# Kernel optimization log

Measured on AMD Instinct MI355X. Metric: run time of the kernel, lower is better.

## Reference

```python
import jax, jax.numpy as jnp
import numpy as np

B, C, D, H = 16, 64, 512, 8
SEQ_LEN, LABEL_LEN, PRED_LEN = 1024, 512, 512
DEC_LEN = LABEL_LEN + PRED_LEN
DFF, KSIZE, FACTOR = 2048, 25, 3
E_LAYERS, D_LAYERS = 2, 1


def _pos_emb(L, d):
    pos = np.arange(L, dtype=np.float32)[:, None]
    div = np.exp(np.arange(0, d, 2, dtype=np.float32) * (-np.log(10000.0) / d))
    pe = np.zeros((L, d), np.float32)
    pe[:, 0::2] = np.sin(pos * div)
    pe[:, 1::2] = np.cos(pos * div)
    return jnp.asarray(pe)


def moving_mean(x, k=KSIZE):
    # AvgPool1d(k, stride=1) with replicate padding of (k-1)//2 at both ends
    pad = (k - 1) // 2
    xp = jnp.concatenate([jnp.repeat(x[:, :1], pad, 1), x, jnp.repeat(x[:, -1:], pad, 1)], axis=1)
    cs = jnp.cumsum(xp, axis=1)
    cs = jnp.concatenate([jnp.zeros_like(cs[:, :1]), cs], axis=1)
    return (cs[:, k:] - cs[:, :-k]) / k


def series_decomp(x):
    mm = moving_mean(x)
    return x - mm, mm


def circ_conv3(x, W):
    # Conv1d kernel=3, circular padding=1, no bias. x [B,L,Cin], W [3,Cin,Cout]
    L = x.shape[1]
    xp = jnp.concatenate([x[:, -1:], x, x[:, :1]], axis=1)
    return sum(jnp.einsum('blc,cd->bld', xp[:, k:k + L], W[k]) for k in range(3))


def my_layernorm(x, g, b):
    # LayerNorm then subtract per-sample mean over the time axis (special seasonal layernorm)
    mu = x.mean(-1, keepdims=True)
    var = x.var(-1, keepdims=True)
    xh = (x - mu) / jnp.sqrt(var + 1e-5) * g + b
    return xh - xh.mean(axis=1, keepdims=True)


def autocorrelation(q, k, v):
    # q,k,v: [B,L,H,E]. FFT cross-correlation, top-k lag selection, time-delay aggregation.
    L = q.shape[1]
    qf = jnp.fft.rfft(q.transpose(0, 2, 3, 1), axis=-1)
    kf = jnp.fft.rfft(k.transpose(0, 2, 3, 1), axis=-1)
    corr = jnp.fft.irfft(qf * jnp.conj(kf), n=L, axis=-1)  # [B,H,E,L]
    top_k = int(FACTOR * np.log(L))
    w, delay = jax.lax.top_k(corr.mean(axis=(1, 2)), top_k)  # [B,K]
    tc = jax.nn.softmax(w, axis=-1)
    vp = v.transpose(0, 2, 3, 1)  # [B,H,E,L]
    base = jnp.arange(L)
    agg = jnp.zeros_like(vp)
    for i in range(top_k):  # small fixed K (= int(factor*log L) = 20)
        idx = (base[None, :] + delay[:, i:i + 1]) % L  # circular shift == gather on doubled values
        pattern = jnp.take_along_axis(vp, idx[:, None, None, :], axis=-1)
        agg = agg + pattern * tc[:, i][:, None, None, None]
    return agg.transpose(0, 3, 1, 2)  # [B,L,H,E]


def ac_layer(q_in, kv_in, Wq, bq, Wk, bk, Wv, bv, Wo, bo):
    Bb, L, _ = q_in.shape
    S = kv_in.shape[1]
    E = D // H
    q = (q_in @ Wq + bq).reshape(Bb, L, H, E)
    k = (kv_in @ Wk + bk).reshape(Bb, S, H, E)
    v = (kv_in @ Wv + bv).reshape(Bb, S, H, E)
    out = autocorrelation(q, k, v)  # L == S by construction here
    return out.reshape(Bb, L, D) @ Wo + bo


def _forward(x_enc, x_dec, enc_emb_w, dec_emb_w, enc_Wq, enc_bq, enc_Wk, enc_bk, enc_Wv, enc_bv, enc_Wo, enc_bo, enc_ff1, enc_ff2, enc_ng, enc_nb, dsa_Wq, dsa_bq, dsa_Wk, dsa_bk, dsa_Wv, dsa_bv, dsa_Wo, dsa_bo, dca_Wq, dca_bq, dca_Wk, dca_bk, dca_Wv, dca_bv, dca_Wo, dca_bo, dec_ff1, dec_ff2, dec_trend_w, proj_w, proj_b):
    mean = jnp.repeat(x_enc.mean(axis=1, keepdims=True), PRED_LEN, axis=1)
    zeros = jnp.zeros((x_dec.shape[0], PRED_LEN, x_dec.shape[2]), x_enc.dtype)
    seasonal_init, trend_init = series_decomp(x_enc)
    trend = jnp.concatenate([trend_init[:, -LABEL_LEN:], mean], axis=1)
    seasonal_init = jnp.concatenate([seasonal_init[:, -LABEL_LEN:], zeros], axis=1)
    # encoder (DataEmbedding_wo_temp = token circular conv + sinusoidal pos, dropout=0)
    x = circ_conv3(x_enc, enc_emb_w) + _pos_emb(SEQ_LEN, D)[None]
    for l in range(E_LAYERS):
        x = x + ac_layer(x, x, enc_Wq[l], enc_bq[l], enc_Wk[l], enc_bk[l], enc_Wv[l], enc_bv[l], enc_Wo[l], enc_bo[l])
        x, _ = series_decomp(x)
        y = jax.nn.gelu(x @ enc_ff1[l], approximate=False) @ enc_ff2[l]
        x, _ = series_decomp(x + y)
    enc_out = my_layernorm(x, enc_ng, enc_nb)
    # decoder
    xd = circ_conv3(seasonal_init, dec_emb_w) + _pos_emb(DEC_LEN, D)[None]
    for l in range(D_LAYERS):
        xd = xd + ac_layer(xd, xd, dsa_Wq[l], dsa_bq[l], dsa_Wk[l], dsa_bk[l], dsa_Wv[l], dsa_bv[l], dsa_Wo[l], dsa_bo[l])
        xd, t1 = series_decomp(xd)
        xd = xd + ac_layer(xd, enc_out, dca_Wq[l], dca_bq[l], dca_Wk[l], dca_bk[l], dca_Wv[l], dca_bv[l], dca_Wo[l], dca_bo[l])
        xd, t2 = series_decomp(xd)
        y = jax.nn.gelu(xd @ dec_ff1[l], approximate=False) @ dec_ff2[l]
        xd, t3 = series_decomp(xd + y)
        trend = trend + circ_conv3(t1 + t2 + t3, dec_trend_w[l])  # trend projection conv
    seasonal = xd @ proj_w + proj_b
    out = trend + seasonal
    return out[:, -PRED_LEN:]


def setup_inputs():
    key = jax.random.key(0)
    ks = iter(jax.random.split(key, 64))
    def n(shape, s=0.02):
        return jax.random.normal(next(ks), shape, jnp.float32) * s
    inp = {}
    inp['x_enc'] = jax.random.normal(next(ks), (B, SEQ_LEN, C), jnp.float32)
    inp['x_dec'] = jax.random.normal(next(ks), (B, DEC_LEN, C), jnp.float32)
    inp['enc_emb_w'] = n((3, C, D))
    inp['dec_emb_w'] = n((3, C, D))
    for p in ['Wq', 'Wk', 'Wv', 'Wo']:
        bp = p.replace('W', 'b')
        inp['enc_' + p] = n((E_LAYERS, D, D)); inp['enc_' + bp] = jnp.zeros((E_LAYERS, D))
        inp['dsa_' + p] = n((D_LAYERS, D, D)); inp['dsa_' + bp] = jnp.zeros((D_LAYERS, D))
        inp['dca_' + p] = n((D_LAYERS, D, D)); inp['dca_' + bp] = jnp.zeros((D_LAYERS, D))
    inp['enc_ff1'] = n((E_LAYERS, D, DFF)); inp['enc_ff2'] = n((E_LAYERS, DFF, D))
    inp['enc_ng'] = jnp.ones((D,), jnp.float32); inp['enc_nb'] = jnp.zeros((D,), jnp.float32)
    inp['dec_ff1'] = n((D_LAYERS, D, DFF)); inp['dec_ff2'] = n((D_LAYERS, DFF, D))
    inp['dec_trend_w'] = n((D_LAYERS, 3, D, C))
    inp['proj_w'] = n((D, C)); inp['proj_b'] = jnp.zeros((C,), jnp.float32)
    return inp


def reference(x_enc, x_dec, enc_emb_w, dec_emb_w, enc_Wq, enc_bq, enc_Wk, enc_bk, enc_Wv, enc_bv, enc_Wo, enc_bo, enc_ff1, enc_ff2, enc_ng, enc_nb, dsa_Wq, dsa_bq, dsa_Wk, dsa_bk, dsa_Wv, dsa_bv, dsa_Wo, dsa_bo, dca_Wq, dca_bq, dca_Wk, dca_bk, dca_Wv, dca_bv, dca_Wo, dca_bo, dec_ff1, dec_ff2, dec_trend_w, proj_w, proj_b):
    return _forward(x_enc, x_dec, enc_emb_w, dec_emb_w, enc_Wq, enc_bq, enc_Wk, enc_bk, enc_Wv, enc_bv, enc_Wo, enc_bo, enc_ff1, enc_ff2, enc_ng, enc_nb, dsa_Wq, dsa_bq, dsa_Wk, dsa_bk, dsa_Wv, dsa_bv, dsa_Wo, dsa_bo, dca_Wq, dca_bq, dca_Wk, dca_bk, dca_Wv, dca_bv, dca_Wo, dca_bo, dec_ff1, dec_ff2, dec_trend_w, proj_w, proj_b)
```

## Files before the change

### kernel.cpp

```cpp
#include <hip/hip_runtime.h>
#include <math.h>

#define B_   16
#define L_   1024
#define C_   64
#define D_   512
#define DFF_ 2048
#define TOPK_ 20

typedef float f4 __attribute__((ext_vector_type(4)));
typedef float f32x4 __attribute__((ext_vector_type(4)));
typedef short bf16x8 __attribute__((ext_vector_type(8)));
typedef unsigned short u16x8 __attribute__((ext_vector_type(8)));

__device__ __forceinline__ unsigned short f2bf(float f) {
    union { float f; unsigned u; } a; a.f = f;
    unsigned r = a.u + 0x7fff + ((a.u >> 16) & 1);
    return (unsigned short)(r >> 16);
}
__device__ __forceinline__ float bf2f(unsigned short h) {
    union { unsigned u; float f; } a; a.u = ((unsigned)h) << 16;
    return a.f;
}

__device__ __forceinline__ float gelu_fast(float c) {
    float z  = c * 0.70710678118654752f;
    float az = fabsf(z);
    float t  = __builtin_amdgcn_rcpf(fmaf(0.3275911f, az, 1.0f));
    float p  = fmaf(fmaf(fmaf(fmaf(1.061405429f, t, -1.453152027f), t,
                              1.421413741f), t, -0.284496736f), t, 0.254829592f) * t;
    float e  = __expf(-z * z);
    float ea = fmaf(-p, e, 1.0f);
    float er = copysignf(ea, z);
    return 0.5f * c * (1.0f + er);
}

__device__ __forceinline__ void gld16(const void* g, void* l) {
    __builtin_amdgcn_global_load_lds(
        (const __attribute__((address_space(1))) unsigned int*)g,
        (__attribute__((address_space(3))) unsigned int*)l, 16, 0, 0);
}


__global__ __launch_bounds__(256)
void gemm_bf16(const unsigned short* __restrict__ A, const unsigned short* __restrict__ Bt,
               float* __restrict__ Cf, unsigned short* __restrict__ Cb,
               unsigned short* __restrict__ Cl,
               const float* __restrict__ bias, int M, int N, int K, int flags, int nx)
{
    __shared__ unsigned short As0[128 * 32], As1[128 * 32];
    __shared__ unsigned short Bs0[128 * 32], Bs1[128 * 32];
    const int tid = threadIdx.x;
    const int wave = tid >> 6, lane = tid & 63;

    int total = gridDim.x;
    int h = blockIdx.x;
    int lidx = h;
    if ((total & 7) == 0) {
        int q = total >> 3;
        lidx = (h & 7) * q + (h >> 3);
    }
    const int bm = (lidx / nx) * 128, bn = (lidx % nx) * 128;
    const int wm = (wave >> 1) << 6, wn = (wave & 1) << 6;

    const int r0 = (wave << 5) + (lane >> 2);
    const int kq = (((lane & 3) ^ ((lane >> 3) & 3)) << 3);
    const unsigned short* Ap0 = A + (size_t)(bm + r0) * K + kq;
    const unsigned short* Ap1 = Ap0 + (size_t)16 * K;
    const unsigned short* Bp0 = Bt + (size_t)(bn + r0) * K + kq;
    const unsigned short* Bp1 = Bp0 + (size_t)16 * K;
    const int wo0 = (wave << 5) * 32, wo1 = ((wave << 5) + 16) * 32;

    const int la = lane & 15, h4 = lane >> 4;
    const int sw = (la >> 1) & 3;
    f32x4 acc[4][4] = {};

    for (int k0 = 0; k0 < K; k0 += 64) {
        gld16(Ap0 + k0, &As0[wo0]);      gld16(Ap1 + k0, &As0[wo1]);
        gld16(Bp0 + k0, &Bs0[wo0]);      gld16(Bp1 + k0, &Bs0[wo1]);
        gld16(Ap0 + k0 + 32, &As1[wo0]); gld16(Ap1 + k0 + 32, &As1[wo1]);
        gld16(Bp0 + k0 + 32, &Bs1[wo0]); gld16(Bp1 + k0 + 32, &Bs1[wo1]);
        __syncthreads();
        bf16x8 a[4], b[4];
#pragma unroll
        for (int i = 0; i < 4; ++i) {
            a[i] = *(const bf16x8*)&As0[(wm + i * 16 + la) * 32 + ((h4 ^ sw) << 3)];
            b[i] = *(const bf16x8*)&Bs0[(wn + i * 16 + la) * 32 + ((h4 ^ sw) << 3)];
        }
#pragma unroll
        for (int mi = 0; mi < 4; ++mi)
#pragma unroll
            for (int ni = 0; ni < 4; ++ni)
                acc[mi][ni] = __builtin_amdgcn_mfma_f32_16x16x32_bf16(a[mi], b[ni], acc[mi][ni], 0, 0, 0);
#pragma unroll
        for (int i = 0; i < 4; ++i) {
            a[i] = *(const bf16x8*)&As1[(wm + i * 16 + la) * 32 + ((h4 ^ sw) << 3)];
            b[i] = *(const bf16x8*)&Bs1[(wn + i * 16 + la) * 32 + ((h4 ^ sw) << 3)];
        }
#pragma unroll
        for (int mi = 0; mi < 4; ++mi)
#pragma unroll
            for (int ni = 0; ni < 4; ++ni)
                acc[mi][ni] = __builtin_amdgcn_mfma_f32_16x16x32_bf16(a[mi], b[ni], acc[mi][ni], 0, 0, 0);
        __syncthreads();
    }

#pragma unroll
    for (int mi = 0; mi < 4; ++mi) {
#pragma unroll
        for (int r = 0; r < 4; ++r) {
            int m = bm + wm + mi * 16 + h4 * 4 + r;
#pragma unroll
            for (int ni = 0; ni < 4; ++ni) {
                int n = bn + wn + ni * 16 + la;
                float c = acc[mi][ni][r];
                if (bias) c += bias[n];
                if (flags & 2) c = gelu_fast(c);
                size_t o = (size_t)m * N + n;
                if (Cf) { if (flags & 1) Cf[o] += c; else Cf[o] = c; }
                if (Cb) {
                    unsigned short hb = f2bf(c);
                    Cb[o] = hb;
                    if (Cl) Cl[o] = f2bf(c - bf2f(hb));
                }
            }
        }
    }
}

__global__ __launch_bounds__(256)
void gemm_split(const unsigned short* __restrict__ A, const unsigned short* __restrict__ Bt,
                unsigned short* __restrict__ o0h, unsigned short* __restrict__ o0l, const float* __restrict__ b0,
                unsigned short* __restrict__ o1h, unsigned short* __restrict__ o1l, const float* __restrict__ b1,
                unsigned short* __restrict__ o2h, unsigned short* __restrict__ o2l, const float* __restrict__ b2,
                float* __restrict__ Gz, int M, int N, int K, int nx)
{
    __shared__ unsigned short As0[128 * 32], As1[128 * 32];
    __shared__ unsigned short Bs0[128 * 32], Bs1[128 * 32];
    const int tid = threadIdx.x;
    const int wave = tid >> 6, lane = tid & 63;

    int total = gridDim.x;
    int h = blockIdx.x;
    if (Gz && h < 64) Gz[h * 256 + tid] = 0.f;
    int lidx = h;
    if ((total & 7) == 0) {
        int q = total >> 3;
        lidx = (h & 7) * q + (h >> 3);
    }
    const int bm = (lidx / nx) * 128, bn = (lidx % nx) * 128;
    const int wm = (wave >> 1) << 6, wn = (wave & 1) << 6;

    const int sel = bn >> 9;
    unsigned short* oh = sel == 0 ? o0h : (sel == 1 ? o1h : o2h);
    unsigned short* ol = sel == 0 ? o0l : (sel == 1 ? o1l : o2l);
    const float* bias  = sel == 0 ? b0  : (sel == 1 ? b1  : b2);
    const int nb = bn & 511;

    const int r0 = (wave << 5) + (lane >> 2);
    const int kq = (((lane & 3) ^ ((lane >> 3) & 3)) << 3);
    const unsigned short* Ap0 = A + (size_t)(bm + r0) * K + kq;
    const unsigned short* Ap1 = Ap0 + (size_t)16 * K;
    const unsigned short* Bp0 = Bt + (size_t)(bn + r0) * K + kq;
    const unsigned short* Bp1 = Bp0 + (size_t)16 * K;
    const int wo0 = (wave << 5) * 32, wo1 = ((wave << 5) + 16) * 32;

    const int la = lane & 15, h4 = lane >> 4;
    const int sw = (la >> 1) & 3;
    f32x4 acc[4][4] = {};

    for (int k0 = 0; k0 < K; k0 += 64) {
        gld16(Ap0 + k0, &As0[wo0]);      gld16(Ap1 + k0, &As0[wo1]);
        gld16(Bp0 + k0, &Bs0[wo0]);      gld16(Bp1 + k0, &Bs0[wo1]);
        gld16(Ap0 + k0 + 32, &As1[wo0]); gld16(Ap1 + k0 + 32, &As1[wo1]);
        gld16(Bp0 + k0 + 32, &Bs1[wo0]); gld16(Bp1 + k0 + 32, &Bs1[wo1]);
        __syncthreads();
        bf16x8 a[4], b[4];
#pragma unroll
        for (int i = 0; i < 4; ++i) {
            a[i] = *(const bf16x8*)&As0[(wm + i * 16 + la) * 32 + ((h4 ^ sw) << 3)];
            b[i] = *(const bf16x8*)&Bs0[(wn + i * 16 + la) * 32 + ((h4 ^ sw) << 3)];
        }
#pragma unroll
        for (int mi = 0; mi < 4; ++mi)
#pragma unroll
            for (int ni = 0; ni < 4; ++ni)
                acc[mi][ni] = __builtin_amdgcn_mfma_f32_16x16x32_bf16(a[mi], b[ni], acc[mi][ni], 0, 0, 0);
#pragma unroll
        for (int i = 0; i < 4; ++i) {
            a[i] = *(const bf16x8*)&As1[(wm + i * 16 + la) * 32 + ((h4 ^ sw) << 3)];
            b[i] = *(const bf16x8*)&Bs1[(wn + i * 16 + la) * 32 + ((h4 ^ sw) << 3)];
        }
#pragma unroll
        for (int mi = 0; mi < 4; ++mi)
#pragma unroll
            for (int ni = 0; ni < 4; ++ni)
                acc[mi][ni] = __builtin_amdgcn_mfma_f32_16x16x32_bf16(a[mi], b[ni], acc[mi][ni], 0, 0, 0);
        __syncthreads();
    }

#pragma unroll
    for (int mi = 0; mi < 4; ++mi) {
#pragma unroll
        for (int r = 0; r < 4; ++r) {
            int m = bm + wm + mi * 16 + h4 * 4 + r;
#pragma unroll
            for (int ni = 0; ni < 4; ++ni) {
                int n2 = nb + wn + ni * 16 + la;
                float c = acc[mi][ni][r] + bias[n2];
                size_t o = (size_t)m * 512 + n2;
                unsigned short hb = f2bf(c);
                oh[o] = hb;
                if (ol) ol[o] = f2bf(c - bf2f(hb));
            }
        }
    }
}

__global__ __launch_bounds__(256)
void tcast_kernel(const float* __restrict__ W, unsigned short* __restrict__ Wt, int R, int Cc)
{
    __shared__ float t[32][33];
    int bx = blockIdx.x * 32, by = blockIdx.y * 32;
    int tx = threadIdx.x & 31, ty = threadIdx.x >> 5;
#pragma unroll
    for (int i = 0; i < 32; i += 8)
        t[ty + i][tx] = W[(size_t)(by + ty + i) * Cc + bx + tx];
    __syncthreads();
#pragma unroll
    for (int i = 0; i < 32; i += 8)
        Wt[(size_t)(bx + ty + i) * R + by + tx] = f2bf(t[tx][ty + i]);
}

struct P16 { const float* p[16]; };
__global__ __launch_bounds__(256)
void tcast_all(P16 srcs, unsigned short* __restrict__ dst)
{
    __shared__ float t[32][33];
    const float* W = srcs.p[blockIdx.z];
    unsigned short* Wt = dst + (size_t)blockIdx.z * 262144;
    int bx = blockIdx.x * 32, by = blockIdx.y * 32;
    int tx = threadIdx.x & 31, ty = threadIdx.x >> 5;
#pragma unroll
    for (int i = 0; i < 32; i += 8)
        t[ty + i][tx] = W[(size_t)(by + ty + i) * 512 + bx + tx];
    __syncthreads();
#pragma unroll
    for (int i = 0; i < 32; i += 8)
        Wt[(size_t)(bx + ty + i) * 512 + by + tx] = f2bf(t[tx][ty + i]);
}

__global__ __launch_bounds__(256)
void emb_kernel(const float* __restrict__ A, const float* __restrict__ W,
                float* __restrict__ Xo, unsigned short* __restrict__ Xb)
{
    __shared__ float As[66][68];
    __shared__ float Ws[3][64][64];
    const int tid = threadIdx.x;
    const int bn = blockIdx.x * 64, bm = blockIdx.y * 64;
    const int base = bm & ~1023;
    for (int i = tid; i < 66 * 64; i += 256) {
        int r = i >> 6, c = i & 63;
        int l = (bm - base) + r - 1;
        if (l < 0) l += 1024; else if (l >= 1024) l -= 1024;
        As[r][c] = A[(size_t)(base + l) * 64 + c];
    }
    for (int i = tid; i < 3 * 64 * 64; i += 256) {
        int tap = i >> 12, rem = i & 4095, k = rem >> 6, c = rem & 63;
        Ws[tap][k][c] = W[((size_t)tap * 64 + k) * 512 + bn + c];
    }
    __syncthreads();
    const int tx = tid & 15, ty = tid >> 4;
    float acc[4][4] = {};
    for (int tap = 0; tap < 3; ++tap)
        for (int k = 0; k < 64; ++k) {
            f4 bv = *(const f4*)&Ws[tap][k][tx * 4];
#pragma unroll
            for (int i = 0; i < 4; ++i) {
                float a = As[ty * 4 + i + tap][k];
#pragma unroll
                for (int j = 0; j < 4; ++j)
                    acc[i][j] = fmaf(a, bv[j], acc[i][j]);
            }
        }
#pragma unroll
    for (int i = 0; i < 4; ++i) {
        int m = bm + ty * 4 + i;
        int l = m & 1023;
#pragma unroll
        for (int j = 0; j < 4; ++j) {
            int n = bn + tx * 4 + j;
            float c = acc[i][j];
            int i2 = n & ~1;
            float div = expf(-(float)i2 * 0.017988946039015984f);
            float ang = (float)l * div;
            c += (n & 1) ? cosf(ang) : sinf(ang);
            size_t o = (size_t)m * 512 + n;
            Xo[o] = c;
            Xb[o] = f2bf(c);
        }
    }
}

__global__ __launch_bounds__(256)
void tail_kernel(const float* __restrict__ TSUM, const float* __restrict__ T1,
                 const float* __restrict__ Wt, const float* __restrict__ pw,
                 float* __restrict__ PC, float* __restrict__ PP)
{
    __shared__ float Ts[18][17];
    __shared__ float T1s[16][17];
    __shared__ float Ws[3][16][64];
    __shared__ float Ps[16][64];
    const int tid = threadIdx.x;
    const int bo = blockIdx.x * 16;
    const int kc = blockIdx.y;
    const int b = bo >> 9;
    const int lbase = (bo & 511) + 512;
    const size_t rowbase = (size_t)b << 10;
    const int tc4 = (tid & 15) * 4;
    const int tr = tid >> 4;
    const int kbeg = kc * 64, kend = kbeg + 64;
    float cacc[4] = {}, pacc[4] = {};

    for (int k0 = kbeg; k0 < kend; k0 += 16) {
        for (int i = tid; i < 18 * 16; i += 256) {
            int r = i >> 4, c = i & 15;
            int l = lbase + r - 1; if (l >= 1024) l -= 1024;
            Ts[r][c] = TSUM[(rowbase + l) * 512 + k0 + c];
        }
        {
            int r = tid >> 4, c = tid & 15;
            T1s[r][c] = T1[(rowbase + lbase + r) * 512 + k0 + c];
        }
        for (int i = tid; i < 3 * 16 * 16; i += 256) {
            int tap = i / 256, rem = i & 255, k = rem >> 4, c4 = (rem & 15) * 4;
            *(f4*)&Ws[tap][k][c4] = *(const f4*)&Wt[((size_t)tap * 512 + k0 + k) * 64 + c4];
        }
        if (tid < 256) {
            int k = tid >> 4, c4 = (tid & 15) * 4;
            *(f4*)&Ps[k][c4] = *(const f4*)&pw[(size_t)(k0 + k) * 64 + c4];
        }
        __syncthreads();
        for (int tap = 0; tap < 3; ++tap)
#pragma unroll
            for (int k = 0; k < 16; ++k) {
                f4 bv = *(const f4*)&Ws[tap][k][tc4];
                float a = Ts[tr + tap][k];
#pragma unroll
                for (int j = 0; j < 4; ++j)
                    cacc[j] = fmaf(a, bv[j], cacc[j]);
            }
#pragma unroll
        for (int k = 0; k < 16; ++k) {
            f4 bv = *(const f4*)&Ps[k][tc4];
            float a = T1s[tr][k];
#pragma unroll
            for (int j = 0; j < 4; ++j)
                pacc[j] = fmaf(a, bv[j], pacc[j]);
        }
        __syncthreads();
    }
    size_t o = ((size_t)kc * 8192 + (bo + tr)) * 64 + tc4;
    *(f4*)&PC[o] = *(f4*)cacc;
    *(f4*)&PP[o] = *(f4*)pacc;
}

__global__ __launch_bounds__(256)
void tailred_kernel(const float* __restrict__ PC, const float* __restrict__ PP,
                    const float* __restrict__ MEANC, const float* __restrict__ pb,
                    float* __restrict__ OUT)
{
    int idx = blockIdx.x * blockDim.x + threadIdx.x;
    int n = idx & 63;
    int b = idx >> 15;
    const size_t S = (size_t)8192 * 64;
    float cs = PC[idx];
    float ps = PP[idx];
#pragma unroll
    for (int s = 1; s < 8; ++s) {
        cs += PC[s * S + idx];
        ps += PP[s * S + idx];
    }
    OUT[idx] = (MEANC[(b << 6) + n] + cs) + (ps + pb[n]);
}

__global__ __launch_bounds__(256)
void corr_mfma(const unsigned short* __restrict__ Qh, const unsigned short* __restrict__ Ql,
               const unsigned short* __restrict__ Kh, const unsigned short* __restrict__ Kl,
               float* __restrict__ G)
{
    __shared__ unsigned short Qhs[128 * 32], Qls[128 * 32], Khs[128 * 32], Kls[128 * 32];
    __shared__ float diagw[4][256];
    const int tid = threadIdx.x;
    const int wave = tid >> 6, lane = tid & 63;

    const int i_ = blockIdx.x;
    const int x_ = i_ & 7, j_ = i_ >> 3;
    const int b = x_ + ((j_ >> 6) << 3);
    const int tile = j_ & 63;
    const int bt = (tile >> 3) * 128, bs = (tile & 7) * 128;

    const int wm = (wave >> 1) << 6, wn = (wave & 1) << 6;
    const size_t boff = (size_t)b << 19;

    const int r0 = (wave << 5) + (lane >> 2);
    const int kq = (((lane & 3) ^ ((lane >> 3) & 3)) << 3);
    const size_t g0 = boff + (size_t)(bt + r0) * 512 + kq;
    const size_t g1 = g0 + (size_t)16 * 512;
    const size_t p0 = boff + (size_t)(bs + r0) * 512 + kq;
    const size_t p1 = p0 + (size_t)16 * 512;
    unsigned short* qh0 = &Qhs[(wave << 5) * 32]; unsigned short* qh1 = &Qhs[((wave << 5) + 16) * 32];
    unsigned short* ql0 = &Qls[(wave << 5) * 32]; unsigned short* ql1 = &Qls[((wave << 5) + 16) * 32];
    unsigned short* kh0 = &Khs[(wave << 5) * 32]; unsigned short* kh1 = &Khs[((wave << 5) + 16) * 32];
    unsigned short* kl0 = &Kls[(wave << 5) * 32]; unsigned short* kl1 = &Kls[((wave << 5) + 16) * 32];

    float* dz = &diagw[0][0];
    dz[tid] = 0.f; dz[tid + 256] = 0.f; dz[tid + 512] = 0.f; dz[tid + 768] = 0.f;

    const int la = lane & 15, h4 = lane >> 4;
    const int sw = (la >> 1) & 3;
    f32x4 acc[4][4] = {};

    for (int k0 = 0; k0 < 512; k0 += 32) {
        gld16(Qh + g0 + k0, qh0); gld16(Qh + g1 + k0, qh1);
        gld16(Ql + g0 + k0, ql0); gld16(Ql + g1 + k0, ql1);
        gld16(Kh + p0 + k0, kh0); gld16(Kh + p1 + k0, kh1);
        gld16(Kl + p0 + k0, kl0); gld16(Kl + p1 + k0, kl1);
        __syncthreads();
        bf16x8 ah[4], al[4], bh[4], bl[4];
#pragma unroll
        for (int i = 0; i < 4; ++i) {
            int ro = (wm + i * 16 + la) * 32 + ((h4 ^ sw) << 3);
            int co = (wn + i * 16 + la) * 32 + ((h4 ^ sw) << 3);
            ah[i] = *(const bf16x8*)&Qhs[ro];
            al[i] = *(const bf16x8*)&Qls[ro];
            bh[i] = *(const bf16x8*)&Khs[co];
            bl[i] = *(const bf16x8*)&Kls[co];
        }
#pragma unroll
        for (int mi = 0; mi < 4; ++mi)
#pragma unroll
            for (int ni = 0; ni < 4; ++ni) {
                acc[mi][ni] = __builtin_amdgcn_mfma_f32_16x16x32_bf16(ah[mi], bh[ni], acc[mi][ni], 0, 0, 0);
                acc[mi][ni] = __builtin_amdgcn_mfma_f32_16x16x32_bf16(ah[mi], bl[ni], acc[mi][ni], 0, 0, 0);
                acc[mi][ni] = __builtin_amdgcn_mfma_f32_16x16x32_bf16(al[mi], bh[ni], acc[mi][ni], 0, 0, 0);
            }
        __syncthreads();
    }

    float rbin[7][4] = {};
#pragma unroll
    for (int mi = 0; mi < 4; ++mi)
#pragma unroll
        for (int ni = 0; ni < 4; ++ni)
#pragma unroll
            for (int r = 0; r < 4; ++r)
                rbin[mi - ni + 3][r] += acc[mi][ni][r];

    const int base = (wm - wn) + 4 * h4 - la + 127;
#pragma unroll
    for (int d = 0; d < 7; ++d)
#pragma unroll
        for (int r = 0; r < 4; ++r)
            atomicAdd(&diagw[wave][base + 16 * (d - 3) + r], rbin[d][r]);
    __syncthreads();
    if (tid < 255) {
        float s = diagw[0][tid] + diagw[1][tid] + diagw[2][tid] + diagw[3][tid];
        int n = (bt - bs + tid - 127) & 1023;
        atomicAdd(&G[(b << 10) + n], s);
    }
}

__global__ __launch_bounds__(256)
void topk_kernel(const float* __restrict__ G, int* __restrict__ delay,
                 float* __restrict__ tc)
{
    __shared__ float vals[1024];
    __shared__ float pw[4];
    __shared__ int   pwi[4];
    __shared__ float wsel[TOPK_];
    __shared__ int   isel[TOPK_];
    const int b = blockIdx.x, tid = threadIdx.x;
    const int lane = tid & 63, wid = tid >> 6;
    for (int i = tid; i < 1024; i += 256) vals[i] = G[(b << 10) + i] * (1.0f / 512.0f);
    __syncthreads();
    for (int it = 0; it < TOPK_; ++it) {
        float bv = -INFINITY; int bi = 0;
#pragma unroll
        for (int u = 0; u < 4; ++u) {
            int i = tid * 4 + u;
            float v = vals[i];
            if (v > bv) { bv = v; bi = i; }
        }
#pragma unroll
        for (int o = 32; o > 0; o >>= 1) {
            float ov = __shfl_xor(bv, o, 64);
            int   oi = __shfl_xor(bi, o, 64);
            if (ov > bv || (ov == bv && oi < bi)) { bv = ov; bi = oi; }
        }
        if (lane == 0) { pw[wid] = bv; pwi[wid] = bi; }
        __syncthreads();
        if (tid == 0) {
            float m = pw[0]; int mi = pwi[0];
#pragma unroll
            for (int t = 1; t < 4; ++t)
                if (pw[t] > m || (pw[t] == m && pwi[t] < mi)) { m = pw[t]; mi = pwi[t]; }
            wsel[it] = m; isel[it] = mi;
            vals[mi] = -INFINITY;
        }
        __syncthreads();
    }
    if (tid == 0) {
        float m = wsel[0];
#pragma unroll
        for (int i = 1; i < TOPK_; ++i) m = fmaxf(m, wsel[i]);
        float e[TOPK_], s = 0.f;
#pragma unroll
        for (int i = 0; i < TOPK_; ++i) { e[i] = expf(wsel[i] - m); s += e[i]; }
        float inv = 1.0f / s;
#pragma unroll
        for (int i = 0; i < TOPK_; ++i) {
            tc[b * TOPK_ + i] = e[i] * inv;
            delay[b * TOPK_ + i] = isel[i];
        }
    }
}

__global__ __launch_bounds__(256)
void agg_kernel(const unsigned short* __restrict__ V, const int* __restrict__ delay,
                const float* __restrict__ tc, unsigned short* __restrict__ out)
{
    __shared__ int   dls[TOPK_];
    __shared__ float tcs[TOPK_];
    int idx = (blockIdx.x * blockDim.x + threadIdx.x) * 8;
    int d = idx & 511;
    int l = (idx >> 9) & 1023;
    int b = idx >> 19;
    if (threadIdx.x < TOPK_) {
        dls[threadIdx.x] = delay[b * TOPK_ + threadIdx.x];
        tcs[threadIdx.x] = tc[b * TOPK_ + threadIdx.x];
    }
    __syncthreads();
    const unsigned short* Vb = V + ((size_t)b << 19);
    float s[8] = {};
#pragma unroll
    for (int i = 0; i < TOPK_; ++i) {
        int row = (l + dls[i]) & 1023;
        float w = tcs[i];
        u16x8 v = *(const u16x8*)&Vb[((size_t)row << 9) + d];
#pragma unroll
        for (int j = 0; j < 8; ++j)
            s[j] = fmaf(w, bf2f(v[j]), s[j]);
    }
    u16x8 o;
#pragma unroll
    for (int j = 0; j < 8; ++j) o[j] = f2bf(s[j]);
    *(u16x8*)&out[idx] = o;
}

__global__ void decomp_kernel(const float* __restrict__ x, float* __restrict__ seas,
                              unsigned short* __restrict__ seasb,
                              float* __restrict__ trend, int Bn, int Ln, int Ch,
                              int nseg, int tmode)
{
    int idx = blockIdx.x * blockDim.x + threadIdx.x;
    int total = Bn * Ch * nseg;
    if (idx >= total) return;
    int ch = idx % Ch;
    int rest = idx / Ch;
    int seg = rest % nseg;
    int b = rest / nseg;
    int segL = Ln / nseg;
    int l0 = seg * segL;
    const float* xp = x + (size_t)b * Ln * Ch + ch;
    float* sp = seas + (size_t)b * Ln * Ch + ch;
    unsigned short* bp = seasb ? seasb + (size_t)b * Ln * Ch + ch : nullptr;
    float* tp = trend ? trend + (size_t)b * Ln * Ch + ch : nullptr;
    float s = 0.f;
    for (int j = -12; j <= 12; ++j) {
        int t = l0 + j;
        t = t < 0 ? 0 : (t > Ln - 1 ? Ln - 1 : t);
        s += xp[(size_t)t * Ch];
    }
    for (int l = l0; l < l0 + segL; ++l) {
        float mm = s * (1.0f / 25.0f);
        float v = xp[(size_t)l * Ch] - mm;
        sp[(size_t)l * Ch] = v;
        if (bp) bp[(size_t)l * Ch] = f2bf(v);
        if (tmode == 1) tp[(size_t)l * Ch] = mm;
        else if (tmode == 2) tp[(size_t)l * Ch] += mm;
        int ta = l + 13; if (ta > Ln - 1) ta = Ln - 1;
        int ts = l - 12; if (ts < 0) ts = 0;
        s += xp[(size_t)ta * Ch] - xp[(size_t)ts * Ch];
    }
}

__global__ __launch_bounds__(256)
void lnrow_kernel(const float* __restrict__ x, const float* __restrict__ g,
                  const float* __restrict__ bv, float* __restrict__ out)
{
    __shared__ float sh1[4], sh2[4];
    int row = blockIdx.x, tid = threadIdx.x;
    const float* xr = x + ((size_t)row << 9);
    float v0 = xr[tid], v1 = xr[tid + 256];
    float s = v0 + v1, q = v0 * v0 + v1 * v1;
#pragma unroll
    for (int o = 32; o > 0; o >>= 1) {
        s += __shfl_down(s, o, 64);
        q += __shfl_down(q, o, 64);
    }
    int wid = tid >> 6;
    if ((tid & 63) == 0) { sh1[wid] = s; sh2[wid] = q; }
    __syncthreads();
    if (tid == 0) {
        sh1[0] = sh1[0] + sh1[1] + sh1[2] + sh1[3];
        sh2[0] = sh2[0] + sh2[1] + sh2[2] + sh2[3];
    }
    __syncthreads();
    float mu = sh1[0] * (1.0f / 512.0f);
    float var = sh2[0] * (1.0f / 512.0f) - mu * mu;
    float inv = rsqrtf(var + 1e-5f);
    out[((size_t)row << 9) + tid] = (v0 - mu) * inv * g[tid] + bv[tid];
    out[((size_t)row << 9) + tid + 256] = (v1 - mu) * inv * g[tid + 256] + bv[tid + 256];
}

__global__ void colmean_kernel(const float* __restrict__ x, float* __restrict__ m)
{
    int idx = blockIdx.x * blockDim.x + threadIdx.x;
    if (idx >= B_ * D_) return;
    int b = idx >> 9, d = idx & 511;
    const float* xp = x + ((size_t)b << 19) + d;
    float s = 0.f;
    for (int l = 0; l < L_; ++l) s += xp[(size_t)l << 9];
    m[idx] = s * (1.0f / 1024.0f);
}

__global__ void colsub_kernel(const float* __restrict__ x, const float* __restrict__ m,
                              unsigned short* __restrict__ out)
{
    int idx = blockIdx.x * blockDim.x + threadIdx.x;
    int d = idx & 511;
    int b = idx >> 19;
    out[idx] = f2bf(x[idx] - m[(b << 9) + d]);
}

__global__ void meanx_kernel(const float* __restrict__ x, float* __restrict__ m)
{
    int idx = blockIdx.x * blockDim.x + threadIdx.x;
    if (idx >= B_ * C_) return;
    int b = idx >> 6, c = idx & 63;
    const float* xp = x + (size_t)b * L_ * C_ + c;
    float s = 0.f;
    for (int l = 0; l < L_; ++l) s += xp[(size_t)l << 6];
    m[idx] = s * (1.0f / 1024.0f);
}

__global__ void builddec_kernel(const float* __restrict__ seenc, float* __restrict__ seasin)
{
    int idx = blockIdx.x * blockDim.x + threadIdx.x;
    int c = idx & 63;
    int l = (idx >> 6) & 1023;
    int b = idx >> 16;
    if (l < 512) {
        int src = (b << 16) + ((512 + l) << 6) + c;
        seasin[idx] = seenc[src];
    } else {
        seasin[idx] = 0.f;
    }
}

extern "C" void kernel_launch(void* const* d_in, const int* in_sizes, int n_in,
                              void* d_out, int out_size, void* d_ws, size_t ws_size,
                              hipStream_t stream)
{
    auto F = [&](int i) { return (const float*)d_in[i]; };
    const float* x_enc     = F(0);
    const float* enc_emb_w = F(2);
    const float* dec_emb_w = F(3);
    const float* enc_Wq = F(4);  const float* enc_bq = F(5);
    const float* dsa_Wq = F(6);  const float* dsa_bq = F(7);
    const float* dca_Wq = F(8);  const float* dca_bq = F(9);
    const float* enc_Wk = F(10); const float* enc_bk = F(11);
    const float* dsa_Wk = F(12); const float* dsa_bk = F(13);
    const float* dca_Wk = F(14); const float* dca_bk = F(15);
    const float* enc_Wv = F(16); const float* enc_bv = F(17);
    const float* dsa_Wv = F(18); const float* dsa_bv = F(19);
    const float* dca_Wv = F(20); const float* dca_bv = F(21);
    const float* enc_Wo = F(22); const float* enc_bo = F(23);
    const float* dsa_Wo = F(24); const float* dsa_bo = F(25);
    const float* dca_Wo = F(26); const float* dca_bo = F(27);
    const float* enc_ff1 = F(28); const float* enc_ff2 = F(29);
    const float* enc_ng = F(30);  const float* enc_nb = F(31);
    const float* dec_ff1 = F(32); const float* dec_ff2 = F(33);
    const float* dec_trend_w = F(34);
    const float* proj_w = F(35);  const float* proj_b = F(36);

    constexpr size_t F512 = (size_t)B_ * L_ * D_;
    constexpr size_t F64  = (size_t)B_ * L_ * C_;
    constexpr size_t SMALL = 1024 + 16384 + 320 + 320 + 8192;
    constexpr size_t WTSA_N = 16 * 262144;
    constexpr size_t WTSF_N = 2 * 1024 * 1024;
    size_t need = (3 * F512 + 2 * F64 + SMALL) * 4 + (8 * F512 + WTSA_N + WTSF_N) * 2;
    if (ws_size < need) return;

    float* X      = (float*)d_ws;
    float* T1     = X + F512;
    float* TSUM   = T1 + F512;
    float* SEASIN = TSUM + F512;
    float* TREND  = SEASIN + F64;
    float* MEANC  = TREND + F64;
    float* G      = MEANC + 1024;
    float* TCW    = G + 16384;
    int*   DEL    = (int*)(TCW + 320);
    float* LNMEAN = (float*)(DEL + 320);
    unsigned short* AB   = (unsigned short*)(LNMEAN + 8192);
    unsigned short* EB   = AB + F512;
    unsigned short* VB   = EB + F512;
    unsigned short* HB   = VB + F512;
    unsigned short* QHI  = HB + F512;
    unsigned short* QLO  = QHI + F512;
    unsigned short* KHI  = QLO + F512;
    unsigned short* KLO  = KHI + F512;
    unsigned short* WTSA = KLO + F512;
    unsigned short* WTSF = WTSA + WTSA_N;
    float* OUT = (float*)d_out;

    const int M = B_ * L_;

    auto mgemm = [&](const unsigned short* A, const unsigned short* Bt, float* Cf,
                     unsigned short* Cb, unsigned short* Cl, const float* bias,
                     int Mm, int Nn, int Kk, int flags) {
        int nx = Nn / 128;
        int total = nx * (Mm / 128);
        gemm_bf16<<<total, 256, 0, stream>>>(A, Bt, Cf, Cb, Cl, bias, Mm, Nn, Kk, flags, nx);
    };
    auto tcast = [&](const float* W, unsigned short* Wt, int R, int Cc) {
        tcast_kernel<<<dim3(Cc / 32, R / 32), 256, 0, stream>>>(W, Wt, R, Cc);
    };
    auto corr_topk_agg = [&]() {
        corr_mfma<<<1024, 256, 0, stream>>>(QHI, QLO, KHI, KLO, G);
        topk_kernel<<<16, 256, 0, stream>>>(G, DEL, TCW);
        agg_kernel<<<(int)(F512 / 8 / 256), 256, 0, stream>>>(VB, DEL, TCW, HB);
    };
    auto attn_self = [&](const unsigned short* xin, int slotbase,
                         const float* bq, const float* bk, const float* bvp, const float* bo,
                         float* resid) {
        gemm_split<<<12 * 128, 256, 0, stream>>>(xin, WTSA + (size_t)slotbase * 262144,
            QHI, QLO, bq, KHI, KLO, bk, VB, nullptr, bvp, G, M, 1536, 512, 12);
        corr_topk_agg();
        mgemm(HB, WTSA + (size_t)(slotbase + 3) * 262144, resid, nullptr, nullptr, bo, M, 512, 512, 1);
    };
    auto attn_cross = [&](const unsigned short* qin, const unsigned short* kvin, int slotbase,
                          const float* bq, const float* bk, const float* bvp, const float* bo,
                          float* resid) {
        mgemm(qin, WTSA + (size_t)slotbase * 262144, nullptr, QHI, QLO, bq, M, 512, 512, 0);
        gemm_split<<<8 * 128, 256, 0, stream>>>(kvin, WTSA + (size_t)(slotbase + 1) * 262144,
            KHI, KLO, bk, VB, nullptr, bvp, nullptr, nullptr, nullptr, G, M, 1024, 512, 8);
        corr_topk_agg();
        mgemm(HB, WTSA + (size_t)(slotbase + 3) * 262144, resid, nullptr, nullptr, bo, M, 512, 512, 1);
    };
    auto ffblock = [&](const unsigned short* xin, const float* W1, const float* W2, float* resid) {
        unsigned short* Wf1 = WTSF;
        unsigned short* Wf2 = WTSF + 1048576;
        unsigned short* HFULL = QHI;
        tcast(W1, Wf1, 512, 2048);
        tcast(W2, Wf2, 2048, 512);
        mgemm(xin, Wf1, nullptr, HFULL, nullptr, nullptr, M, 2048, 512, 2);
        mgemm(HFULL, Wf2, resid, nullptr, nullptr, nullptr, M, 512, 2048, 1);
    };

    {
        P16 srcs;
        for (int l = 0; l < 2; ++l) {
            srcs.p[l * 4 + 0] = enc_Wq + (size_t)l * 262144;
            srcs.p[l * 4 + 1] = enc_Wk + (size_t)l * 262144;
            srcs.p[l * 4 + 2] = enc_Wv + (size_t)l * 262144;
            srcs.p[l * 4 + 3] = enc_Wo + (size_t)l * 262144;
        }
        srcs.p[8]  = dsa_Wq; srcs.p[9]  = dsa_Wk; srcs.p[10] = dsa_Wv; srcs.p[11] = dsa_Wo;
        srcs.p[12] = dca_Wq; srcs.p[13] = dca_Wk; srcs.p[14] = dca_Wv; srcs.p[15] = dca_Wo;
        tcast_all<<<dim3(16, 16, 16), 256, 0, stream>>>(srcs, WTSA);
    }

    float* SEENC = (float*)QHI;
    decomp_kernel<<<(B_ * C_ * 64 + 255) / 256, 256, 0, stream>>>(x_enc, SEENC, nullptr, nullptr, B_, L_, C_, 64, 0);
    meanx_kernel<<<(B_ * C_ + 255) / 256, 256, 0, stream>>>(x_enc, MEANC);
    builddec_kernel<<<(int)(F64 / 256), 256, 0, stream>>>(SEENC, SEASIN);

    emb_kernel<<<dim3(8, 256), 256, 0, stream>>>(x_enc, enc_emb_w, X, AB);

    for (int l = 0; l < 2; ++l) {
        attn_self(AB, l * 4,
                  enc_bq + l * D_, enc_bk + l * D_, enc_bv + l * D_, enc_bo + l * D_, X);
        decomp_kernel<<<(B_ * D_ * 64 + 255) / 256, 256, 0, stream>>>(X, T1, AB, nullptr, B_, L_, D_, 64, 0);
        ffblock(AB, enc_ff1 + (size_t)l * D_ * DFF_, enc_ff2 + (size_t)l * DFF_ * D_, T1);
        decomp_kernel<<<(B_ * D_ * 64 + 255) / 256, 256, 0, stream>>>(T1, X, AB, nullptr, B_, L_, D_, 64, 0);
    }
    lnrow_kernel<<<M, 256, 0, stream>>>(X, enc_ng, enc_nb, T1);
    colmean_kernel<<<(B_ * D_ + 255) / 256, 256, 0, stream>>>(T1, LNMEAN);
    colsub_kernel<<<(int)(F512 / 256), 256, 0, stream>>>(T1, LNMEAN, EB);

    float* XD = X;
    emb_kernel<<<dim3(8, 256), 256, 0, stream>>>(SEASIN, dec_emb_w, XD, AB);

    attn_self(AB, 8, dsa_bq, dsa_bk, dsa_bv, dsa_bo, XD);
    decomp_kernel<<<(B_ * D_ * 64 + 255) / 256, 256, 0, stream>>>(XD, T1, AB, TSUM, B_, L_, D_, 64, 1);

    attn_cross(AB, EB, 12, dca_bq, dca_bk, dca_bv, dca_bo, T1);
    decomp_kernel<<<(B_ * D_ * 64 + 255) / 256, 256, 0, stream>>>(T1, XD, AB, TSUM, B_, L_, D_, 64, 2);

    ffblock(AB, dec_ff1, dec_ff2, XD);
    decomp_kernel<<<(B_ * D_ * 64 + 255) / 256, 256, 0, stream>>>(XD, T1, nullptr, TSUM, B_, L_, D_, 64, 2);

    float* PART_C = (float*)QHI;
    float* PART_P = PART_C + (size_t)8 * 8192 * 64;
    tail_kernel<<<dim3(512, 8), 256, 0, stream>>>(TSUM, T1, dec_trend_w, proj_w, PART_C, PART_P);
    tailred_kernel<<<2048, 256, 0, stream>>>(PART_C, PART_P, MEANC, proj_b, OUT);
}
```

Measured before the change: 1.859 ms.

## Precompute positional embedding table and remap block order in agg/decomp kernels

Adds a kernel that writes the sinusoidal positional embedding table (1024x512) into a workspace buffer once, and the embedding kernel now reads that table instead of evaluating expf/sinf/cosf per output element. The agg and decomp kernels also permute their block index so that consecutive hardware block IDs, which are likely dispatched round-robin across XCDs, map to contiguous chunks of work. This is meant to improve cache locality on the multi-die GPU. It costs an extra kernel launch plus a 2 MB table read per embedding, and it reuses the unused TREND workspace slot.

```diff
diff --git a/kernel.cpp b/kernel.cpp
--- a/kernel.cpp
+++ b/kernel.cpp
@@ -251,7 +251,19 @@
 }
 
 __global__ __launch_bounds__(256)
+void pegen_kernel(float* __restrict__ PE)
+{
+    int idx = blockIdx.x * blockDim.x + threadIdx.x;
+    int n = idx & 511, l = idx >> 9;
+    int i2 = n & ~1;
+    float div = expf(-(float)i2 * 0.017988946039015984f);
+    float ang = (float)l * div;
+    PE[idx] = (n & 1) ? cosf(ang) : sinf(ang);
+}
+
+__global__ __launch_bounds__(256)
 void emb_kernel(const float* __restrict__ A, const float* __restrict__ W,
+                const float* __restrict__ PEt,
                 float* __restrict__ Xo, unsigned short* __restrict__ Xb)
 {
     __shared__ float As[66][68];
@@ -290,11 +302,7 @@
 #pragma unroll
         for (int j = 0; j < 4; ++j) {
             int n = bn + tx * 4 + j;
-            float c = acc[i][j];
-            int i2 = n & ~1;
-            float div = expf(-(float)i2 * 0.017988946039015984f);
-            float ang = (float)l * div;
-            c += (n & 1) ? cosf(ang) : sinf(ang);
+            float c = acc[i][j] + PEt[((size_t)l << 9) + n];
             size_t o = (size_t)m * 512 + n;
             Xo[o] = c;
             Xb[o] = f2bf(c);
@@ -532,7 +540,12 @@
 {
     __shared__ int   dls[TOPK_];
     __shared__ float tcs[TOPK_];
-    int idx = (blockIdx.x * blockDim.x + threadIdx.x) * 8;
+    int h = blockIdx.x, g = gridDim.x, lh = h;
+    if ((g & 7) == 0) {
+        int q = g >> 3;
+        lh = (h & 7) * q + (h >> 3);
+    }
+    int idx = (lh * blockDim.x + threadIdx.x) * 8;
     int d = idx & 511;
     int l = (idx >> 9) & 1023;
     int b = idx >> 19;
@@ -563,7 +576,12 @@
                               float* __restrict__ trend, int Bn, int Ln, int Ch,
                               int nseg, int tmode)
 {
-    int idx = blockIdx.x * blockDim.x + threadIdx.x;
+    int h = blockIdx.x, g = gridDim.x, lh = h;
+    if ((g & 7) == 0) {
+        int q = g >> 3;
+        lh = (h & 7) * q + (h >> 3);
+    }
+    int idx = lh * blockDim.x + threadIdx.x;
     int total = Bn * Ch * nseg;
     if (idx >= total) return;
     int ch = idx % Ch;
@@ -707,8 +725,8 @@
     float* T1     = X + F512;
     float* TSUM   = T1 + F512;
     float* SEASIN = TSUM + F512;
-    float* TREND  = SEASIN + F64;
-    float* MEANC  = TREND + F64;
+    float* PET    = SEASIN + F64;
+    float* MEANC  = PET + F64;
     float* G      = MEANC + 1024;
     float* TCW    = G + 16384;
     int*   DEL    = (int*)(TCW + 320);
@@ -781,13 +799,14 @@
         srcs.p[12] = dca_Wq; srcs.p[13] = dca_Wk; srcs.p[14] = dca_Wv; srcs.p[15] = dca_Wo;
         tcast_all<<<dim3(16, 16, 16), 256, 0, stream>>>(srcs, WTSA);
     }
+    pegen_kernel<<<2048, 256, 0, stream>>>(PET);
 
     float* SEENC = (float*)QHI;
     decomp_kernel<<<(B_ * C_ * 64 + 255) / 256, 256, 0, stream>>>(x_enc, SEENC, nullptr, nullptr, B_, L_, C_, 64, 0);
     meanx_kernel<<<(B_ * C_ + 255) / 256, 256, 0, stream>>>(x_enc, MEANC);
     builddec_kernel<<<(int)(F64 / 256), 256, 0, stream>>>(SEENC, SEASIN);
 
-    emb_kernel<<<dim3(8, 256), 256, 0, stream>>>(x_enc, enc_emb_w, X, AB);
+    emb_kernel<<<dim3(8, 256), 256, 0, stream>>>(x_enc, enc_emb_w, PET, X, AB);
 
     for (int l = 0; l < 2; ++l) {
         attn_self(AB, l * 4,
@@ -801,7 +820,7 @@
     colsub_kernel<<<(int)(F512 / 256), 256, 0, stream>>>(T1, LNMEAN, EB);
 
     float* XD = X;
-    emb_kernel<<<dim3(8, 256), 256, 0, stream>>>(SEASIN, dec_emb_w, XD, AB);
+    emb_kernel<<<dim3(8, 256), 256, 0, stream>>>(SEASIN, dec_emb_w, PET, XD, AB);
 
     attn_self(AB, 8, dsa_bq, dsa_bk, dsa_bv, dsa_bo, XD);
     decomp_kernel<<<(B_ * D_ * 64 + 255) / 256, 256, 0, stream>>>(XD, T1, AB, TSUM, B_, L_, D_, 64, 1);
```

Measured after the change: 1.793 ms. 3.6% less time.
